# Kernel optimization log

Measured on AMD Instinct MI355X. Metric: run time of the kernel, lower is better.

## Reference

```python
import jax, jax.numpy as jnp
import numpy as np

N = 50000      # nodes
E = 800000     # edges (avg degree 16)
H = 128        # hidden_channels
F = 128        # num_filters
G = 50         # num_gaussians
L = 6          # num_interactions
CUT = 10.0     # cutoff
H2 = H // 2
OUT = 12


def ssp(x):
    # ShiftedSoftplus: softplus(x) - log(2)
    return jax.nn.softplus(x) - jnp.log(2.0)


def setup_inputs() -> dict:
    key = jax.random.key(0)
    ks = jax.random.split(key, 16)
    s = 0.05
    x_atoms = jax.random.randint(ks[0], (N,), 0, 100)
    edge_index = jax.random.randint(ks[1], (2, E), 0, N)
    edge_attr = jax.random.uniform(ks[2], (E,), minval=0.05, maxval=CUT)
    return {
        "x_atoms": x_atoms,
        "edge_index": edge_index,
        "edge_attr": edge_attr,
        "embedding": jax.random.normal(ks[3], (100, H)) * s,
        # per-interaction stacked params [L, ...]
        "mlp_w1": jax.random.normal(ks[4], (L, G, F)) * s,
        "mlp_b1": jnp.zeros((L, F)),
        "mlp_w2": jax.random.normal(ks[5], (L, F, F)) * s,
        "mlp_b2": jnp.zeros((L, F)),
        "conv1_w": jax.random.normal(ks[6], (L, H, F)) * s,   # CFConv.lin1 (no bias)
        "conv2_w": jax.random.normal(ks[7], (L, F, H)) * s,   # CFConv.lin2
        "conv2_b": jnp.zeros((L, H)),
        "int_lin_w": jax.random.normal(ks[8], (L, H, H)) * s,  # InteractionBlock.lin
        "int_lin_b": jnp.zeros((L, H)),
        # head
        "lin1_w": jax.random.normal(ks[9], (H, H2)) * s,
        "lin1_b": jnp.zeros((H2,)),
        "lin2_w": jax.random.normal(ks[10], (H2, H2)) * s,
        "lin2_b": jnp.zeros((H2,)),
        "readout_w": jax.random.normal(ks[11], (H2, OUT)) * s,
        "readout_b": jnp.zeros((OUT,)),
    }


def reference(x_atoms, edge_index, edge_attr, embedding,
              mlp_w1, mlp_b1, mlp_w2, mlp_b2,
              conv1_w, conv2_w, conv2_b, int_lin_w, int_lin_b,
              lin1_w, lin1_b, lin2_w, lin2_b, readout_w, readout_b):
    h = embedding[x_atoms]  # [N, H]

    # Gaussian smearing of distances -> [E, G]
    offset = jnp.linspace(0.0, CUT, G)
    coeff = -0.5 / (offset[1] - offset[0]) ** 2
    ed = jnp.exp(coeff * (edge_attr[:, None] - offset) ** 2)

    # cosine cutoff weight per edge
    C = 0.5 * (jnp.cos(edge_attr * jnp.pi / CUT) + 1.0)  # [E]

    src = edge_index[0]
    dst = edge_index[1]

    for l in range(L):
        # filter network on expanded distances -> [E, F]
        W = ssp(ed @ mlp_w1[l] + mlp_b1[l]) @ mlp_w2[l] + mlp_b2[l]
        W = W * C[:, None]
        xf = h @ conv1_w[l]                     # [N, F]
        msg = xf[src] * W                        # gather + modulate, [E, F]
        agg = jax.ops.segment_sum(msg, dst, num_segments=N)  # scatter-add, [N, F]
        v = agg @ conv2_w[l] + conv2_b[l]        # [N, H]
        v = ssp(v)
        v = v @ int_lin_w[l] + int_lin_b[l]
        h = h + v                                # residual

    h = ssp(h @ lin1_w + lin1_b)
    h = h @ lin2_w + lin2_b
    h_agg = jnp.sum(h, axis=0, keepdims=True)    # [1, H2]
    return h_agg @ readout_w + readout_b         # [1, OUT]
```

## Files before the change

kernel.cpp:

```cpp
#include <hip/hip_runtime.h>
#include <hip/hip_bf16.h>
#include <math.h>

#define NN 50000
#define EE 800000
#define HH 128
#define FF 128
#define GG 50
#define LL 6
#define H2D 64
#define OUT_DIM 12
#define NK 4096
#define NBLK 782
#define SB 196
#define NBUK 196

typedef __bf16 bf16;
typedef __attribute__((ext_vector_type(8))) __bf16 bf16x8;
typedef __attribute__((ext_vector_type(4))) __bf16 bf16x4;
typedef __attribute__((ext_vector_type(4))) float f32x4;
typedef __attribute__((ext_vector_type(4))) unsigned u32x4;

#define DEV __device__ __forceinline__

DEV float sspf(float x) {
    return fmaxf(x, 0.f) + __logf(1.f + __expf(-fabsf(x))) - 0.69314718055994531f;
}

DEV f32x4 mfma16(bf16x8 a, bf16x8 b, f32x4 c) {
    return __builtin_amdgcn_mfma_f32_16x16x32_bf16(a, b, c, 0, 0, 0);
}

DEV float blo(unsigned u) { return __uint_as_float(u << 16); }
DEV float bhi(unsigned u) { return __uint_as_float(u & 0xffff0000u); }

struct PrepArgs {
    const float *conv1_w, *conv2_w, *int_lin_w, *mlp_w1, *mlp_w2, *lin1_w, *lin2_w;
    bf16 *c1t, *c2t, *ilt, *w1t, *w2t, *l1t, *l2t;
    int* hist;
};

__global__ void prep_kernel(PrepArgs p) {
    int j = blockIdx.x;
    for (int i = blockIdx.x * 256 + threadIdx.x; i < NN; i += 32 * 256) p.hist[i] = 0;
    const float* src = nullptr; bf16* dst = nullptr; int R = 0, C = 0, K = 0;
    if (j < 30) {
        int l = j / 5, m = j % 5;
        switch (m) {
            case 0: src = p.conv1_w + l * HH * FF;   dst = p.c1t + l * FF * HH;  R = HH; C = FF; K = HH; break;
            case 1: src = p.conv2_w + l * FF * HH;   dst = p.c2t + l * HH * FF;  R = FF; C = HH; K = FF; break;
            case 2: src = p.int_lin_w + l * HH * HH; dst = p.ilt + l * HH * HH;  R = HH; C = HH; K = HH; break;
            case 3: src = p.mlp_w1 + l * GG * FF;    dst = p.w1t + l * FF * 64;  R = GG; C = FF; K = 64; break;
            case 4: src = p.mlp_w2 + l * FF * FF;    dst = p.w2t + l * FF * FF;  R = FF; C = FF; K = FF; break;
        }
    } else if (j == 30) { src = p.lin1_w; dst = p.l1t; R = HH;  C = H2D; K = HH; }
    else                { src = p.lin2_w; dst = p.l2t; R = H2D; C = H2D; K = H2D; }
    int total = C * K;
    for (int idx = threadIdx.x; idx < total; idx += blockDim.x) {
        int c = idx / K, r = idx - c * K;
        dst[idx] = (r < R) ? (bf16)src[r * C + c] : (bf16)0.f;
    }
}

__global__ __launch_bounds__(256) void table_kernel(const bf16* __restrict__ w1t,
                                                    const bf16* __restrict__ w2t,
                                                    const float* __restrict__ mlp_b1,
                                                    const float* __restrict__ mlp_b2,
                                                    bf16* __restrict__ tab) {
    __shared__ bf16 sW1[128 * 72];
    __shared__ bf16 sW2[128 * 136];
    __shared__ bf16 sT1[64 * 136];
    int tid = threadIdx.x;
    int l = blockIdx.x / 65, rb = blockIdx.x % 65;
    const bf16* W1 = w1t + (size_t)l * 128 * 64;
    const bf16* W2 = w2t + (size_t)l * 128 * 128;
    for (int idx = tid * 8; idx < 128 * 64; idx += 2048) {
        int n = idx >> 6, k = idx & 63;
        *(bf16x8*)&sW1[n * 72 + k] = *(const bf16x8*)(W1 + idx);
    }
    for (int idx = tid * 8; idx < 128 * 128; idx += 2048) {
        int n = idx >> 7, k = idx & 127;
        *(bf16x8*)&sW2[n * 136 + k] = *(const bf16x8*)(W2 + idx);
    }
    int w = tid >> 6, lane = tid & 63, ln = lane & 15, kg = lane >> 4;
    int rowt = rb * 64 + w * 16;
    float d1 = (float)min(rowt + ln, NK) * (10.f / NK);
    const float step = 10.f / 49.f;
    const float coeff = -0.5f / (step * step);
    __syncthreads();
    f32x4 acc[8] = {};
#pragma unroll
    for (int k0 = 0; k0 < 64; k0 += 32) {
        bf16x8 a;
#pragma unroll
        for (int jj = 0; jj < 8; jj++) {
            int g = k0 + kg * 8 + jj;
            float diff = d1 - g * step;
            float v = (g < GG) ? __expf(coeff * diff * diff) : 0.f;
            a[jj] = (bf16)v;
        }
#pragma unroll
        for (int t = 0; t < 8; t++) {
            bf16x8 b = *(const bf16x8*)&sW1[(t * 16 + ln) * 72 + k0 + kg * 8];
            acc[t] = mfma16(a, b, acc[t]);
        }
    }
    const float* b1 = mlp_b1 + l * FF;
#pragma unroll
    for (int t = 0; t < 8; t++) {
        int colt = t * 16 + ln;
        float bb = b1[colt];
#pragma unroll
        for (int r = 0; r < 4; r++)
            sT1[(w * 16 + kg * 4 + r) * 136 + colt] = (bf16)sspf(acc[t][r] + bb);
    }
    __syncthreads();
    f32x4 acc2[8] = {};
#pragma unroll
    for (int k0 = 0; k0 < 128; k0 += 32) {
        bf16x8 a = *(const bf16x8*)&sT1[(w * 16 + ln) * 136 + k0 + kg * 8];
#pragma unroll
        for (int t = 0; t < 8; t++) {
            bf16x8 b = *(const bf16x8*)&sW2[(t * 16 + ln) * 136 + k0 + kg * 8];
            acc2[t] = mfma16(a, b, acc2[t]);
        }
    }
    const float* b2 = mlp_b2 + l * FF;
    float Cw[4]; int rrow[4];
#pragma unroll
    for (int r = 0; r < 4; r++) {
        int rr = rowt + kg * 4 + r;
        rrow[r] = rr;
        float dd = (float)min(rr, NK) * (10.f / NK);
        Cw[r] = 0.5f * (cosf(dd * 0.31415926535897932f) + 1.f);
    }
#pragma unroll
    for (int t = 0; t < 8; t++) {
        int colt = t * 16 + ln;
        float bb = b2[colt];
#pragma unroll
        for (int r = 0; r < 4; r++) {
            if (rrow[r] <= NK)
                tab[((size_t)l * (NK + 1) + rrow[r]) * FF + colt] = (bf16)((acc2[t][r] + bb) * Cw[r]);
        }
    }
}

__global__ void hist_kernel(const int* __restrict__ eidx, int* __restrict__ hist) {
    int e = blockIdx.x * 256 + threadIdx.x;
    if (e < EE) atomicAdd(&hist[eidx[EE + e]], 1);
}

__global__ __launch_bounds__(256) void scanA_kernel(const int* __restrict__ hist,
                                                    int* __restrict__ bsum) {
    __shared__ int red[256];
    int t = threadIdx.x;
    int i = blockIdx.x * 256 + t;
    int v = (i < NN) ? hist[i] : 0;
    red[t] = v;
    __syncthreads();
    for (int off = 128; off > 0; off >>= 1) {
        if (t < off) red[t] += red[t + off];
        __syncthreads();
    }
    if (t == 0) bsum[blockIdx.x] = red[0];
}

__global__ __launch_bounds__(256) void scanB_kernel(int* __restrict__ bsum) {
    __shared__ int buf[256];
    int t = threadIdx.x;
    int v = (t < SB) ? bsum[t] : 0;
    buf[t] = v;
    __syncthreads();
    for (int off = 1; off < 256; off <<= 1) {
        int y = (t >= off) ? buf[t - off] : 0;
        __syncthreads();
        buf[t] += y;
        __syncthreads();
    }
    if (t < SB) bsum[t] = buf[t] - v;
}

__global__ __launch_bounds__(256) void scanC_kernel(const int* __restrict__ hist,
                                                    const int* __restrict__ bsum,
                                                    int* __restrict__ rs,
                                                    int* __restrict__ bucket_cur) {
    __shared__ int buf[256];
    int t = threadIdx.x;
    int i = blockIdx.x * 256 + t;
    int v = (i < NN) ? hist[i] : 0;
    buf[t] = v;
    __syncthreads();
    for (int off = 1; off < 256; off <<= 1) {
        int y = (t >= off) ? buf[t - off] : 0;
        __syncthreads();
        buf[t] += y;
        __syncthreads();
    }
    if (i < NN) {
        int ex = buf[t] - v + bsum[blockIdx.x];
        rs[i] = ex;
        if ((i & 255) == 0) bucket_cur[i >> 8] = ex;
    }
}

__global__ __launch_bounds__(256) void scat1_kernel(const float* __restrict__ eattr,
                                                    const int* __restrict__ eidx,
                                                    int* __restrict__ bucket_cur,
                                                    int2* __restrict__ tmp8) {
    __shared__ int cnt[NBUK];
    __shared__ int res[NBUK];
    int t = threadIdx.x;
    for (int i = t; i < NBUK; i += 256) cnt[i] = 0;
    __syncthreads();
    int e0 = blockIdx.x * 4096;
    int pv[16], dd[16], bk[16];
#pragma unroll
    for (int i = 0; i < 16; i++) {
        int e = e0 + i * 256 + t;
        if (e < EE) {
            int d = eidx[EE + e];
            int k = (int)(eattr[e] * ((float)NK / 10.f) + 0.5f);
            k = min(k, NK);
            pv[i] = k | (eidx[e] << 13);
            dd[i] = d;
            bk[i] = d >> 8;
            atomicAdd(&cnt[bk[i]], 1);
        } else bk[i] = -1;
    }
    __syncthreads();
    for (int i = t; i < NBUK; i += 256) {
        int c = cnt[i];
        res[i] = (c > 0) ? atomicAdd(&bucket_cur[i], c) : 0;
        cnt[i] = 0;
    }
    __syncthreads();
#pragma unroll
    for (int i = 0; i < 16; i++) {
        if (bk[i] >= 0) {
            int rank = atomicAdd(&cnt[bk[i]], 1);
            int2 v; v.x = pv[i]; v.y = dd[i];
            tmp8[res[bk[i]] + rank] = v;
        }
    }
}

__global__ __launch_bounds__(256) void scat2_kernel(const int* __restrict__ rs,
                                                    const int2* __restrict__ tmp8,
                                                    int* __restrict__ es) {
    __shared__ int off[256];
    __shared__ int loc[256];
    int b = blockIdx.x, t = threadIdx.x;
    int nb0 = b * 256;
    int nnb = min(256, NN - nb0);
    int base = rs[nb0];
    int end = (nb0 + 256 < NN) ? rs[nb0 + 256] : EE;
    loc[t] = 0;
    if (t < nnb) off[t] = rs[nb0 + t] - base;
    __syncthreads();
    for (int e = base + t; e < end; e += 256) {
        int2 v = tmp8[e];
        int nl = v.y - nb0;
        int rank = atomicAdd(&loc[nl], 1);
        es[base + off[nl] + rank] = v.x;
    }
}

__global__ __launch_bounds__(256) void xf0_kernel(const int* __restrict__ x_atoms,
                                                  const float* __restrict__ emb,
                                                  const bf16* __restrict__ c1t,
                                                  bf16* __restrict__ hb,
                                                  bf16* __restrict__ xf) {
    __shared__ bf16 sB[128 * 136];
    int tid = threadIdx.x;
    for (int idx = tid * 8; idx < 128 * 128; idx += 2048) {
        int n = idx >> 7, k = idx & 127;
        *(bf16x8*)&sB[n * 136 + k] = *(const bf16x8*)(c1t + idx);
    }
    int w = tid >> 6, lane = tid & 63, ln = lane & 15, kg = lane >> 4;
    int rowt = blockIdx.x * 64 + w * 16;
    int nrow = rowt + ln;
    int arow = min(nrow, NN - 1);
    bool rowok = nrow < NN;
    int atom = x_atoms[arow];
    __syncthreads();
    f32x4 acc[8] = {};
#pragma unroll
    for (int k0 = 0; k0 < 128; k0 += 32) {
        const float* ep = emb + (size_t)atom * HH + k0 + kg * 8;
        f32x4 u0 = *(const f32x4*)ep;
        f32x4 u1 = *(const f32x4*)(ep + 4);
        bf16x8 a;
#pragma unroll
        for (int q = 0; q < 4; q++) { a[q] = (bf16)u0[q]; a[q + 4] = (bf16)u1[q]; }
        if (rowok) *(bf16x8*)(hb + (size_t)nrow * HH + k0 + kg * 8) = a;
#pragma unroll
        for (int t = 0; t < 8; t++) {
            bf16x8 b = *(const bf16x8*)&sB[(t * 16 + ln) * 136 + k0 + kg * 8];
            acc[t] = mfma16(a, b, acc[t]);
        }
    }
#pragma unroll
    for (int t = 0; t < 8; t++) {
        int colt = t * 16 + ln;
#pragma unroll
        for (int r = 0; r < 4; r++) {
            int orow = rowt + kg * 4 + r;
            if (orow < NN) xf[orow * FF + colt] = (bf16)acc[t][r];
        }
    }
}

__global__ __launch_bounds__(256) void edge_kernel(const int* __restrict__ es,
                                                   const int* __restrict__ rs,
                                                   const int* __restrict__ hist,
                                                   const bf16* __restrict__ xf,
                                                   const bf16* __restrict__ tab,
                                                   bf16* __restrict__ aggb) {
    int tid = threadIdx.x;
    int w = tid >> 6, lane = tid & 63;
    int q = lane >> 4, cl = lane & 15;
    int n = blockIdx.x * 4 + w;
    int start = rs[n], deg = hist[n];
    float a0 = 0.f, a1 = 0.f, a2 = 0.f, a3 = 0.f;
    float a4 = 0.f, a5 = 0.f, a6 = 0.f, a7 = 0.f;
    for (int base = 0; base < deg; base += 64) {
        int cnt = min(deg - base, 64);
        int pv = (lane < cnt) ? es[start + base + lane] : 0;
        int iters = (cnt + 7) >> 3;
#pragma unroll 2
        for (int j = 0; j < iters; j++) {
            int j0 = 8 * j + q;
            int j1 = j0 + 4;
            bool va = j0 < cnt, vb = j1 < cnt;
            int v0 = __shfl(pv, j0);
            int v1 = __shfl(pv, j1);
            int ka = v0 & 8191, sa = v0 >> 13;
            int kb = v1 & 8191, sb1 = v1 >> 13;
            u32x4 tpa = *(const u32x4*)(tab + (size_t)ka * FF + 8 * cl);
            u32x4 xua = *(const u32x4*)(xf + (size_t)sa * FF + 8 * cl);
            u32x4 tpb = *(const u32x4*)(tab + (size_t)kb * FF + 8 * cl);
            u32x4 xub = *(const u32x4*)(xf + (size_t)sb1 * FF + 8 * cl);
            unsigned ta0 = va ? tpa.x : 0u;
            unsigned ta1 = va ? tpa.y : 0u;
            unsigned ta2 = va ? tpa.z : 0u;
            unsigned ta3 = va ? tpa.w : 0u;
            unsigned tb0 = vb ? tpb.x : 0u;
            unsigned tb1 = vb ? tpb.y : 0u;
            unsigned tb2 = vb ? tpb.z : 0u;
            unsigned tb3 = vb ? tpb.w : 0u;
            a0 = fmaf(blo(ta0), blo(xua.x), a0);
            a1 = fmaf(bhi(ta0), bhi(xua.x), a1);
            a2 = fmaf(blo(ta1), blo(xua.y), a2);
            a3 = fmaf(bhi(ta1), bhi(xua.y), a3);
            a4 = fmaf(blo(ta2), blo(xua.z), a4);
            a5 = fmaf(bhi(ta2), bhi(xua.z), a5);
            a6 = fmaf(blo(ta3), blo(xua.w), a6);
            a7 = fmaf(bhi(ta3), bhi(xua.w), a7);
            a0 = fmaf(blo(tb0), blo(xub.x), a0);
            a1 = fmaf(bhi(tb0), bhi(xub.x), a1);
            a2 = fmaf(blo(tb1), blo(xub.y), a2);
            a3 = fmaf(bhi(tb1), bhi(xub.y), a3);
            a4 = fmaf(blo(tb2), blo(xub.z), a4);
            a5 = fmaf(bhi(tb2), bhi(xub.z), a5);
            a6 = fmaf(blo(tb3), blo(xub.w), a6);
            a7 = fmaf(bhi(tb3), bhi(xub.w), a7);
        }
    }
    a0 += __shfl_xor(a0, 16); a0 += __shfl_xor(a0, 32);
    a1 += __shfl_xor(a1, 16); a1 += __shfl_xor(a1, 32);
    a2 += __shfl_xor(a2, 16); a2 += __shfl_xor(a2, 32);
    a3 += __shfl_xor(a3, 16); a3 += __shfl_xor(a3, 32);
    a4 += __shfl_xor(a4, 16); a4 += __shfl_xor(a4, 32);
    a5 += __shfl_xor(a5, 16); a5 += __shfl_xor(a5, 32);
    a6 += __shfl_xor(a6, 16); a6 += __shfl_xor(a6, 32);
    a7 += __shfl_xor(a7, 16); a7 += __shfl_xor(a7, 32);
    if (q == 0) {
        bf16x8 pk;
        pk[0] = (bf16)a0; pk[1] = (bf16)a1; pk[2] = (bf16)a2; pk[3] = (bf16)a3;
        pk[4] = (bf16)a4; pk[5] = (bf16)a5; pk[6] = (bf16)a6; pk[7] = (bf16)a7;
        *(bf16x8*)(aggb + (size_t)n * FF + 8 * cl) = pk;
    }
}

__global__ __launch_bounds__(256) void update_kernel(const bf16* __restrict__ aggb,
                                                     const bf16* __restrict__ c2t,
                                                     const float* __restrict__ c2b,
                                                     const bf16* __restrict__ ilt,
                                                     const float* __restrict__ ilb,
                                                     bf16* __restrict__ hb,
                                                     const bf16* __restrict__ c1n,
                                                     bf16* __restrict__ xf_out,
                                                     const bf16* __restrict__ l1t,
                                                     const float* __restrict__ l1b,
                                                     const bf16* __restrict__ l2t,
                                                     const float* __restrict__ l2b,
                                                     float* __restrict__ partial) {
    __shared__ bf16 sB[64 * 136];
    __shared__ bf16 sT[64 * 136];
    int tid = threadIdx.x;
    int w = tid >> 6, lane = tid & 63, ln = lane & 15, kg = lane >> 4;
    int rowt = blockIdx.x * 64 + w * 16;
    int nrow = rowt + ln;
    int arow = min(nrow, NN - 1);
    bool rowok = nrow < NN;
    bf16x4 hpre[8];
#pragma unroll
    for (int t = 0; t < 8; t++)
        hpre[t] = *(const bf16x4*)(hb + (size_t)arow * HH + t * 16 + kg * 4);
    bf16x8 breg[4];
#pragma unroll
    for (int k0 = 0; k0 < 4; k0++)
        breg[k0] = *(const bf16x8*)(aggb + (size_t)arow * FF + k0 * 32 + kg * 8);

    f32x4 acc[8] = {};
#pragma unroll
    for (int h = 0; h < 2; h++) {
        __syncthreads();
        for (int idx = tid * 8; idx < 64 * 128; idx += 2048)
            *(bf16x8*)&sB[(idx >> 7) * 136 + (idx & 127)] =
                *(const bf16x8*)(c2t + h * 64 * 128 + idx);
        __syncthreads();
#pragma unroll
        for (int k0 = 0; k0 < 128; k0 += 32) {
#pragma unroll
            for (int t = 0; t < 4; t++) {
                bf16x8 afrag = *(const bf16x8*)&sB[(t * 16 + ln) * 136 + k0 + kg * 8];
                acc[h * 4 + t] = mfma16(afrag, breg[k0 >> 5], acc[h * 4 + t]);
            }
        }
    }
#pragma unroll
    for (int t = 0; t < 8; t++) {
        f32x4 bb = *(const f32x4*)(c2b + t * 16 + kg * 4);
        bf16x4 pk;
#pragma unroll
        for (int r = 0; r < 4; r++) pk[r] = (bf16)sspf(acc[t][r] + bb[r]);
        *(bf16x4*)&sT[(w * 16 + ln) * 136 + t * 16 + kg * 4] = pk;
    }
    f32x4 acc2[8] = {};
#pragma unroll
    for (int h = 0; h < 2; h++) {
        __syncthreads();
        for (int idx = tid * 8; idx < 64 * 128; idx += 2048)
            *(bf16x8*)&sB[(idx >> 7) * 136 + (idx & 127)] =
                *(const bf16x8*)(ilt + h * 64 * 128 + idx);
        __syncthreads();
#pragma unroll
        for (int k0 = 0; k0 < 128; k0 += 32) {
            bf16x8 bfrag = *(const bf16x8*)&sT[(w * 16 + ln) * 136 + k0 + kg * 8];
#pragma unroll
            for (int t = 0; t < 4; t++) {
                bf16x8 afrag = *(const bf16x8*)&sB[(t * 16 + ln) * 136 + k0 + kg * 8];
                acc2[h * 4 + t] = mfma16(afrag, bfrag, acc2[h * 4 + t]);
            }
        }
    }
    bool is_last = (c1n == nullptr);
#pragma unroll
    for (int t = 0; t < 8; t++) {
        f32x4 bb = *(const f32x4*)(ilb + t * 16 + kg * 4);
        bf16x4 pk;
#pragma unroll
        for (int r = 0; r < 4; r++)
            pk[r] = (bf16)((float)hpre[t][r] + acc2[t][r] + bb[r]);
        if (rowok && !is_last) *(bf16x4*)(hb + (size_t)nrow * HH + t * 16 + kg * 4) = pk;
        *(bf16x4*)&sT[(w * 16 + ln) * 136 + t * 16 + kg * 4] = pk;
    }
    if (!is_last) {
        f32x4 acc3[8] = {};
#pragma unroll
        for (int h = 0; h < 2; h++) {
            __syncthreads();
            for (int idx = tid * 8; idx < 64 * 128; idx += 2048)
                *(bf16x8*)&sB[(idx >> 7) * 136 + (idx & 127)] =
                    *(const bf16x8*)(c1n + h * 64 * 128 + idx);
            __syncthreads();
#pragma unroll
            for (int k0 = 0; k0 < 128; k0 += 32) {
                bf16x8 bfrag = *(const bf16x8*)&sT[(w * 16 + ln) * 136 + k0 + kg * 8];
#pragma unroll
                for (int t = 0; t < 4; t++) {
                    bf16x8 afrag = *(const bf16x8*)&sB[(t * 16 + ln) * 136 + k0 + kg * 8];
                    acc3[h * 4 + t] = mfma16(afrag, bfrag, acc3[h * 4 + t]);
                }
            }
        }
#pragma unroll
        for (int t = 0; t < 8; t++) {
            bf16x4 pk;
#pragma unroll
            for (int r = 0; r < 4; r++) pk[r] = (bf16)acc3[t][r];
            if (rowok) *(bf16x4*)(xf_out + (size_t)nrow * FF + t * 16 + kg * 4) = pk;
        }
    } else {
        __syncthreads();
        for (int idx = tid * 8; idx < 64 * 128; idx += 2048)
            *(bf16x8*)&sB[(idx >> 7) * 136 + (idx & 127)] = *(const bf16x8*)(l1t + idx);
        __syncthreads();
        f32x4 acch[4] = {};
#pragma unroll
        for (int k0 = 0; k0 < 128; k0 += 32) {
            bf16x8 a = *(const bf16x8*)&sT[(w * 16 + ln) * 136 + k0 + kg * 8];
#pragma unroll
            for (int t = 0; t < 4; t++) {
                bf16x8 b = *(const bf16x8*)&sB[(t * 16 + ln) * 136 + k0 + kg * 8];
                acch[t] = mfma16(a, b, acch[t]);
            }
        }
#pragma unroll
        for (int t = 0; t < 4; t++) {
            int colt = t * 16 + ln;
            float bb = l1b[colt];
#pragma unroll
            for (int r = 0; r < 4; r++)
                sT[(w * 16 + kg * 4 + r) * 136 + colt] = (bf16)sspf(acch[t][r] + bb);
        }
        __syncthreads();
        for (int idx = tid * 8; idx < 64 * 64; idx += 2048) {
            int n = idx >> 6, k = idx & 63;
            *(bf16x8*)&sB[n * 136 + k] = *(const bf16x8*)(l2t + idx);
        }
        __syncthreads();
        f32x4 acc2h[4] = {};
#pragma unroll
        for (int k0 = 0; k0 < 64; k0 += 32) {
            bf16x8 a = *(const bf16x8*)&sT[(w * 16 + ln) * 136 + k0 + kg * 8];
#pragma unroll
            for (int t = 0; t < 4; t++) {
                bf16x8 b = *(const bf16x8*)&sB[(t * 16 + ln) * 136 + k0 + kg * 8];
                acc2h[t] = mfma16(a, b, acc2h[t]);
            }
        }
        __syncthreads();
        float* sPart = (float*)sT;
#pragma unroll
        for (int t = 0; t < 4; t++) {
            int colt = t * 16 + ln;
            float bb = l2b[colt];
            float v = 0.f;
#pragma unroll
            for (int r = 0; r < 4; r++) {
                int orow = rowt + kg * 4 + r;
                if (orow < NN) v += acc2h[t][r] + bb;
            }
            v += __shfl_xor(v, 16);
            v += __shfl_xor(v, 32);
            if (kg == 0) sPart[w * 64 + colt] = v;
        }
        __syncthreads();
        if (tid < 64) {
            float s = sPart[tid] + sPart[64 + tid] + sPart[128 + tid] + sPart[192 + tid];
            partial[blockIdx.x * 64 + tid] = s;
        }
    }
}

__global__ __launch_bounds__(256) void finalA_kernel(const float* __restrict__ partial,
                                                     float* __restrict__ colsum) {
    __shared__ float red[256];
    int c = blockIdx.x, t = threadIdx.x;
    float s = 0.f;
    for (int b = t; b < NBLK; b += 256) s += partial[b * 64 + c];
    red[t] = s;
    __syncthreads();
    for (int off = 128; off > 0; off >>= 1) {
        if (t < off) red[t] += red[t + off];
        __syncthreads();
    }
    if (t == 0) colsum[c] = red[0];
}

__global__ __launch_bounds__(64) void finalB_kernel(const float* __restrict__ colsum,
                                                    const float* __restrict__ rw,
                                                    const float* __restrict__ rb,
                                                    float* __restrict__ out) {
    __shared__ float sv[64];
    int j = threadIdx.x;
    sv[j] = colsum[j];
    __syncthreads();
    if (j < OUT_DIM) {
        float o = rb[j];
        for (int i = 0; i < H2D; i++) o += sv[i] * rw[i * OUT_DIM + j];
        out[j] = o;
    }
}

extern "C" void kernel_launch(void* const* d_in, const int* in_sizes, int n_in,
                              void* d_out, int out_size, void* d_ws, size_t ws_size,
                              hipStream_t stream) {
    const int*   x_atoms    = (const int*)d_in[0];
    const int*   edge_index = (const int*)d_in[1];
    const float* edge_attr  = (const float*)d_in[2];
    const float* embedding  = (const float*)d_in[3];
    const float* mlp_w1     = (const float*)d_in[4];
    const float* mlp_b1     = (const float*)d_in[5];
    const float* mlp_w2     = (const float*)d_in[6];
    const float* mlp_b2     = (const float*)d_in[7];
    const float* conv1_w    = (const float*)d_in[8];
    const float* conv2_w    = (const float*)d_in[9];
    const float* conv2_b    = (const float*)d_in[10];
    const float* int_lin_w  = (const float*)d_in[11];
    const float* int_lin_b  = (const float*)d_in[12];
    const float* lin1_w     = (const float*)d_in[13];
    const float* lin1_b     = (const float*)d_in[14];
    const float* lin2_w     = (const float*)d_in[15];
    const float* lin2_b     = (const float*)d_in[16];
    const float* readout_w  = (const float*)d_in[17];
    const float* readout_b  = (const float*)d_in[18];

    char* ws = (char*)d_ws;
    bf16*  hb      = (bf16*)(ws + 0);
    bf16*  xfA     = (bf16*)(ws + 12800000);
    bf16*  xfB     = (bf16*)(ws + 25600000);
    bf16*  aggb    = (bf16*)(ws + 38400000);
    float* partial = (float*)(ws + 51200000);
    size_t wb = 51400192;
    bf16* c1t = (bf16*)(ws + wb);
    bf16* c2t = (bf16*)(ws + wb + 196608);
    bf16* ilt = (bf16*)(ws + wb + 393216);
    bf16* w1t = (bf16*)(ws + wb + 589824);
    bf16* w2t = (bf16*)(ws + wb + 688128);
    bf16* l1t = (bf16*)(ws + wb + 884736);
    bf16* l2t = (bf16*)(ws + wb + 901120);
    int*   d_hist = (int*)(ws + 52309504);
    int*   d_rs   = (int*)(ws + 52509504);
    int*   d_bcur = (int*)(ws + 52709504);
    int*   d_bsum = (int*)(ws + 52710528);
    int*   d_es   = (int*)(ws + 52711552);
    bf16*  tab    = (bf16*)(ws + 55911552);
    int2*  d_tmp8 = (int2*)(ws + 62204544);
    float* colsum = (float*)(ws + 68604544);

    PrepArgs pa = { conv1_w, conv2_w, int_lin_w, mlp_w1, mlp_w2, lin1_w, lin2_w,
                    c1t, c2t, ilt, w1t, w2t, l1t, l2t, d_hist };
    prep_kernel<<<32, 256, 0, stream>>>(pa);
    table_kernel<<<LL * 65, 256, 0, stream>>>(w1t, w2t, mlp_b1, mlp_b2, tab);

    hist_kernel<<<(EE + 255) / 256, 256, 0, stream>>>(edge_index, d_hist);
    scanA_kernel<<<SB, 256, 0, stream>>>(d_hist, d_bsum);
    scanB_kernel<<<1, 256, 0, stream>>>(d_bsum);
    scanC_kernel<<<SB, 256, 0, stream>>>(d_hist, d_bsum, d_rs, d_bcur);
    scat1_kernel<<<NBUK, 256, 0, stream>>>(edge_attr, edge_index, d_bcur, d_tmp8);
    scat2_kernel<<<NBUK, 256, 0, stream>>>(d_rs, d_tmp8, d_es);

    xf0_kernel<<<NBLK, 256, 0, stream>>>(x_atoms, embedding, c1t, hb, xfA);
    bf16* xf_in = xfA;
    bf16* xf_out = xfB;
    for (int l = 0; l < LL; l++) {
        edge_kernel<<<NN / 4, 256, 0, stream>>>(d_es, d_rs, d_hist, xf_in,
                                                tab + (size_t)l * (NK + 1) * FF, aggb);
        const bf16* c1n = (l + 1 < LL) ? (c1t + (size_t)(l + 1) * FF * HH) : nullptr;
        update_kernel<<<NBLK, 256, 0, stream>>>(aggb, c2t + (size_t)l * HH * FF,
                                                conv2_b + l * HH,
                                                ilt + (size_t)l * HH * HH, int_lin_b + l * HH,
                                                hb, c1n, xf_out,
                                                l1t, lin1_b, l2t, lin2_b, partial);
        bf16* tmp = xf_in; xf_in = xf_out; xf_out = tmp;
    }
    finalA_kernel<<<64, 256, 0, stream>>>(partial, colsum);
    finalB_kernel<<<1, 64, 0, stream>>>(colsum, readout_w, readout_b, (float*)d_out);
}
```

Measured before the change: 542.6 us.

## Double update_kernel rows per block and merge scanB into scanC

The update kernel now runs 512 threads over 128 rows per block, so each block loads the shared weight tiles once for twice as many rows. The aggregated inputs are staged through shared memory and B fragments are kept in registers across the k-loop. The separate scanB launch is removed: each scanC block reduces the preceding block sums itself. This cuts weight reloads and one launch, but raises shared memory and register use per block and may lower occupancy.

```diff
diff --git a/kernel.cpp b/kernel.cpp
--- a/kernel.cpp
+++ b/kernel.cpp
@@ -12,6 +12,7 @@
 #define OUT_DIM 12
 #define NK 4096
 #define NBLK 782
+#define NB2 391
 #define SB 196
 #define NBUK 196
 
@@ -166,31 +167,23 @@
     if (t == 0) bsum[blockIdx.x] = red[0];
 }
 
-__global__ __launch_bounds__(256) void scanB_kernel(int* __restrict__ bsum) {
-    __shared__ int buf[256];
-    int t = threadIdx.x;
-    int v = (t < SB) ? bsum[t] : 0;
-    buf[t] = v;
-    __syncthreads();
-    for (int off = 1; off < 256; off <<= 1) {
-        int y = (t >= off) ? buf[t - off] : 0;
-        __syncthreads();
-        buf[t] += y;
-        __syncthreads();
-    }
-    if (t < SB) bsum[t] = buf[t] - v;
-}
-
 __global__ __launch_bounds__(256) void scanC_kernel(const int* __restrict__ hist,
                                                     const int* __restrict__ bsum,
                                                     int* __restrict__ rs,
                                                     int* __restrict__ bucket_cur) {
     __shared__ int buf[256];
+    __shared__ int bbuf[256];
     int t = threadIdx.x;
     int i = blockIdx.x * 256 + t;
     int v = (i < NN) ? hist[i] : 0;
     buf[t] = v;
-    __syncthreads();
+    bbuf[t] = (t < SB && t < blockIdx.x) ? bsum[t] : 0;
+    __syncthreads();
+    for (int off = 128; off > 0; off >>= 1) {
+        if (t < off) bbuf[t] += bbuf[t + off];
+        __syncthreads();
+    }
+    int base = bbuf[0];
     for (int off = 1; off < 256; off <<= 1) {
         int y = (t >= off) ? buf[t - off] : 0;
         __syncthreads();
@@ -198,7 +191,7 @@
         __syncthreads();
     }
     if (i < NN) {
-        int ex = buf[t] - v + bsum[blockIdx.x];
+        int ex = buf[t] - v + base;
         rs[i] = ex;
         if ((i & 255) == 0) bucket_cur[i >> 8] = ex;
     }
@@ -383,7 +376,7 @@
     }
 }
 
-__global__ __launch_bounds__(256) void update_kernel(const bf16* __restrict__ aggb,
+__global__ __launch_bounds__(512) void update_kernel(const bf16* __restrict__ aggb,
                                                      const bf16* __restrict__ c2t,
                                                      const float* __restrict__ c2b,
                                                      const bf16* __restrict__ ilt,
@@ -397,10 +390,10 @@
                                                      const float* __restrict__ l2b,
                                                      float* __restrict__ partial) {
     __shared__ bf16 sB[64 * 136];
-    __shared__ bf16 sT[64 * 136];
+    __shared__ bf16 sT[128 * 136];
     int tid = threadIdx.x;
     int w = tid >> 6, lane = tid & 63, ln = lane & 15, kg = lane >> 4;
-    int rowt = blockIdx.x * 64 + w * 16;
+    int rowt = blockIdx.x * 128 + w * 16;
     int nrow = rowt + ln;
     int arow = min(nrow, NN - 1);
     bool rowok = nrow < NN;
@@ -408,19 +401,28 @@
 #pragma unroll
     for (int t = 0; t < 8; t++)
         hpre[t] = *(const bf16x4*)(hb + (size_t)arow * HH + t * 16 + kg * 4);
+    {
+        int srow = min(rowt + (lane >> 2), NN - 1);
+        const bf16* src = aggb + (size_t)srow * FF + (lane & 3) * 32;
+        bf16* dstp = &sT[(w * 16 + (lane >> 2)) * 136 + (lane & 3) * 32];
+#pragma unroll
+        for (int j = 0; j < 4; j++)
+            *(bf16x8*)(dstp + j * 8) = *(const bf16x8*)(src + j * 8);
+    }
+    f32x4 acc[8] = {};
     bf16x8 breg[4];
 #pragma unroll
-    for (int k0 = 0; k0 < 4; k0++)
-        breg[k0] = *(const bf16x8*)(aggb + (size_t)arow * FF + k0 * 32 + kg * 8);
-
-    f32x4 acc[8] = {};
-#pragma unroll
     for (int h = 0; h < 2; h++) {
-        __syncthreads();
-        for (int idx = tid * 8; idx < 64 * 128; idx += 2048)
+        if (h) __syncthreads();
+        for (int idx = tid * 8; idx < 64 * 128; idx += 4096)
             *(bf16x8*)&sB[(idx >> 7) * 136 + (idx & 127)] =
                 *(const bf16x8*)(c2t + h * 64 * 128 + idx);
         __syncthreads();
+        if (h == 0) {
+#pragma unroll
+            for (int k0 = 0; k0 < 4; k0++)
+                breg[k0] = *(const bf16x8*)&sT[(w * 16 + ln) * 136 + k0 * 32 + kg * 8];
+        }
 #pragma unroll
         for (int k0 = 0; k0 < 128; k0 += 32) {
 #pragma unroll
@@ -439,20 +441,25 @@
         *(bf16x4*)&sT[(w * 16 + ln) * 136 + t * 16 + kg * 4] = pk;
     }
     f32x4 acc2[8] = {};
+    bf16x8 breg2[4];
 #pragma unroll
     for (int h = 0; h < 2; h++) {
         __syncthreads();
-        for (int idx = tid * 8; idx < 64 * 128; idx += 2048)
+        for (int idx = tid * 8; idx < 64 * 128; idx += 4096)
             *(bf16x8*)&sB[(idx >> 7) * 136 + (idx & 127)] =
                 *(const bf16x8*)(ilt + h * 64 * 128 + idx);
         __syncthreads();
+        if (h == 0) {
+#pragma unroll
+            for (int k0 = 0; k0 < 4; k0++)
+                breg2[k0] = *(const bf16x8*)&sT[(w * 16 + ln) * 136 + k0 * 32 + kg * 8];
+        }
 #pragma unroll
         for (int k0 = 0; k0 < 128; k0 += 32) {
-            bf16x8 bfrag = *(const bf16x8*)&sT[(w * 16 + ln) * 136 + k0 + kg * 8];
 #pragma unroll
             for (int t = 0; t < 4; t++) {
                 bf16x8 afrag = *(const bf16x8*)&sB[(t * 16 + ln) * 136 + k0 + kg * 8];
-                acc2[h * 4 + t] = mfma16(afrag, bfrag, acc2[h * 4 + t]);
+                acc2[h * 4 + t] = mfma16(afrag, breg2[k0 >> 5], acc2[h * 4 + t]);
             }
         }
     }
@@ -469,20 +476,25 @@
     }
     if (!is_last) {
         f32x4 acc3[8] = {};
+        bf16x8 breg3[4];
 #pragma unroll
         for (int h = 0; h < 2; h++) {
             __syncthreads();
-            for (int idx = tid * 8; idx < 64 * 128; idx += 2048)
+            for (int idx = tid * 8; idx < 64 * 128; idx += 4096)
                 *(bf16x8*)&sB[(idx >> 7) * 136 + (idx & 127)] =
                     *(const bf16x8*)(c1n + h * 64 * 128 + idx);
             __syncthreads();
+            if (h == 0) {
+#pragma unroll
+                for (int k0 = 0; k0 < 4; k0++)
+                    breg3[k0] = *(const bf16x8*)&sT[(w * 16 + ln) * 136 + k0 * 32 + kg * 8];
+            }
 #pragma unroll
             for (int k0 = 0; k0 < 128; k0 += 32) {
-                bf16x8 bfrag = *(const bf16x8*)&sT[(w * 16 + ln) * 136 + k0 + kg * 8];
 #pragma unroll
                 for (int t = 0; t < 4; t++) {
                     bf16x8 afrag = *(const bf16x8*)&sB[(t * 16 + ln) * 136 + k0 + kg * 8];
-                    acc3[h * 4 + t] = mfma16(afrag, bfrag, acc3[h * 4 + t]);
+                    acc3[h * 4 + t] = mfma16(afrag, breg3[k0 >> 5], acc3[h * 4 + t]);
                 }
             }
         }
@@ -495,7 +507,7 @@
         }
     } else {
         __syncthreads();
-        for (int idx = tid * 8; idx < 64 * 128; idx += 2048)
+        for (int idx = tid * 8; idx < 64 * 128; idx += 4096)
             *(bf16x8*)&sB[(idx >> 7) * 136 + (idx & 127)] = *(const bf16x8*)(l1t + idx);
         __syncthreads();
         f32x4 acch[4] = {};
@@ -517,7 +529,7 @@
                 sT[(w * 16 + kg * 4 + r) * 136 + colt] = (bf16)sspf(acch[t][r] + bb);
         }
         __syncthreads();
-        for (int idx = tid * 8; idx < 64 * 64; idx += 2048) {
+        for (int idx = tid * 8; idx < 64 * 64; idx += 4096) {
             int n = idx >> 6, k = idx & 63;
             *(bf16x8*)&sB[n * 136 + k] = *(const bf16x8*)(l2t + idx);
         }
@@ -550,7 +562,9 @@
         }
         __syncthreads();
         if (tid < 64) {
-            float s = sPart[tid] + sPart[64 + tid] + sPart[128 + tid] + sPart[192 + tid];
+            float s = 0.f;
+#pragma unroll
+            for (int ww = 0; ww < 8; ww++) s += sPart[ww * 64 + tid];
             partial[blockIdx.x * 64 + tid] = s;
         }
     }
@@ -561,7 +575,7 @@
     __shared__ float red[256];
     int c = blockIdx.x, t = threadIdx.x;
     float s = 0.f;
-    for (int b = t; b < NBLK; b += 256) s += partial[b * 64 + c];
+    for (int b = t; b < NB2; b += 256) s += partial[b * 64 + c];
     red[t] = s;
     __syncthreads();
     for (int off = 128; off > 0; off >>= 1) {
@@ -639,7 +653,6 @@
 
     hist_kernel<<<(EE + 255) / 256, 256, 0, stream>>>(edge_index, d_hist);
     scanA_kernel<<<SB, 256, 0, stream>>>(d_hist, d_bsum);
-    scanB_kernel<<<1, 256, 0, stream>>>(d_bsum);
     scanC_kernel<<<SB, 256, 0, stream>>>(d_hist, d_bsum, d_rs, d_bcur);
     scat1_kernel<<<NBUK, 256, 0, stream>>>(edge_attr, edge_index, d_bcur, d_tmp8);
     scat2_kernel<<<NBUK, 256, 0, stream>>>(d_rs, d_tmp8, d_es);
@@ -651,11 +664,11 @@
         edge_kernel<<<NN / 4, 256, 0, stream>>>(d_es, d_rs, d_hist, xf_in,
                                                 tab + (size_t)l * (NK + 1) * FF, aggb);
         const bf16* c1n = (l + 1 < LL) ? (c1t + (size_t)(l + 1) * FF * HH) : nullptr;
-        update_kernel<<<NBLK, 256, 0, stream>>>(aggb, c2t + (size_t)l * HH * FF,
-                                                conv2_b + l * HH,
-                                                ilt + (size_t)l * HH * HH, int_lin_b + l * HH,
-                                                hb, c1n, xf_out,
-                                                l1t, lin1_b, l2t, lin2_b, partial);
+        update_kernel<<<NB2, 512, 0, stream>>>(aggb, c2t + (size_t)l * HH * FF,
+                                               conv2_b + l * HH,
+                                               ilt + (size_t)l * HH * HH, int_lin_b + l * HH,
+                                               hb, c1n, xf_out,
+                                               l1t, lin1_b, l2t, lin2_b, partial);
         bf16* tmp = xf_in; xf_in = xf_out; xf_out = tmp;
     }
     finalA_kernel<<<64, 256, 0, stream>>>(partial, colsum);
```

Result: no change. 539.9 us (-0.5%).
